# Kernel tuning notes

Measured on AMD Instinct MI355X. Metric: run time of the kernel, lower is better.

## Reference

```python
import jax, jax.numpy as jnp
import numpy as np

T, H, I, R, Z, K = 4096, 1024, 512, 32, 8, 4
E = R + Z
CAP = 768  # per-expert capacity; mean load = T*K/E = 409.6, CAP is ~18 sigma above mean


def setup_inputs() -> dict:
    key = jax.random.key(0)
    k1, k2, k3, k4, k5 = jax.random.split(key, 5)
    hidden_states = jax.random.normal(k1, (T, H), jnp.float32)
    top_k_index = jax.random.randint(k2, (T, K), 0, E).astype(jnp.int64)
    top_k_weights = jax.random.uniform(k3, (T, K), jnp.float32)
    gate_up_proj = jax.random.normal(k4, (E, 2 * I, H), jnp.float32) * 0.02
    down_proj = jax.random.normal(k5, (R, H, I), jnp.float32) * 0.02
    return {
        "hidden_states": hidden_states,
        "top_k_index": top_k_index,
        "top_k_weights": top_k_weights,
        "gate_up_proj": gate_up_proj,
        "down_proj": down_proj,
    }


def reference(hidden_states, top_k_index, top_k_weights, gate_up_proj, down_proj):
    n_tok, h = hidden_states.shape
    k = top_k_index.shape[1]
    n_routed = down_proj.shape[0]
    n_total = gate_up_proj.shape[0]
    A = n_tok * k  # total assignments

    flat_e = top_k_index.reshape(-1).astype(jnp.int32)          # [A]
    flat_t = jnp.repeat(jnp.arange(n_tok, dtype=jnp.int32), k)  # [A]
    flat_w = top_k_weights.reshape(-1)                          # [A]

    # ---- zero experts: weighted identity ----
    zero_w = jnp.sum(jnp.where(top_k_index >= n_routed, top_k_weights, 0.0), axis=1)
    out = hidden_states * zero_w[:, None]

    # ---- routed experts via capacity-buffer grouped GEMM ----
    order = jnp.argsort(flat_e)  # stable sort groups assignments by expert
    se = flat_e[order]
    st = flat_t[order]
    sw = flat_w[order]

    counts = jnp.bincount(flat_e, length=n_total)        # [E]
    starts = jnp.cumsum(counts) - counts                 # exclusive cumsum
    pos = jnp.arange(A, dtype=jnp.int32) - starts[se].astype(jnp.int32)  # slot within expert

    valid = (se < n_routed) & (pos < CAP)
    e_idx = jnp.where(valid, se, 0)
    p_idx = jnp.where(valid, pos, 0)

    xs = jnp.where(valid[:, None], hidden_states[st], 0.0)   # [A,H]
    xbuf = jnp.zeros((n_routed, CAP, h), hidden_states.dtype).at[e_idx, p_idx].add(xs)

    # grouped gated MLP: F.linear(x, W) == x @ W.T with W [out,in]
    gu = jnp.einsum('ech,eoh->eco', xbuf, gate_up_proj[:n_routed])  # [R,CAP,2I]
    gate, up = jnp.split(gu, 2, axis=-1)
    mid = jax.nn.silu(gate) * up                                    # [R,CAP,I]
    ybuf = jnp.einsum('eci,ehi->ech', mid, down_proj)               # [R,CAP,H]

    ya = ybuf[e_idx, p_idx] * jnp.where(valid, sw, 0.0)[:, None]    # [A,H]
    out = out.at[st].add(ya)
    return out
```

## Files before the change

kernel.cpp:

```cpp
#include <hip/hip_runtime.h>
#include <stdint.h>

#define NT 4096
#define HD 1024
#define ID 512
#define RE 32
#define EE 40
#define KT 4
#define CAPACITY 768

typedef __bf16 bf16x8 __attribute__((ext_vector_type(8)));
typedef float f32x4 __attribute__((ext_vector_type(4)));
typedef unsigned int u32x4 __attribute__((ext_vector_type(4)));
typedef unsigned short u16x4 __attribute__((ext_vector_type(4)));

__device__ __forceinline__ float bf2f(unsigned short u) {
    union { unsigned int i; float f; } v; v.i = ((unsigned int)u) << 16; return v.f;
}
__device__ __forceinline__ unsigned short f2bf(float f) {
    union { float f; unsigned int i; } v; v.f = f;
    unsigned int u = v.i;
    return (unsigned short)((u + 0x7fffu + ((u >> 16) & 1u)) >> 16);
}

__device__ __forceinline__ u32x4 ld8(const void* p, size_t ei, int inF32) {
    if (!inF32) {
        return *(const u32x4*)((const unsigned short*)p + ei);
    } else {
        const float* f = (const float*)p + ei;
        f32x4 a = *(const f32x4*)f;
        f32x4 b = *(const f32x4*)(f + 4);
        u32x4 r;
        r[0] = (unsigned)f2bf(a[0]) | ((unsigned)f2bf(a[1]) << 16);
        r[1] = (unsigned)f2bf(a[2]) | ((unsigned)f2bf(a[3]) << 16);
        r[2] = (unsigned)f2bf(b[0]) | ((unsigned)f2bf(b[1]) << 16);
        r[3] = (unsigned)f2bf(b[2]) | ((unsigned)f2bf(b[3]) << 16);
        return r;
    }
}

__global__ __launch_bounds__(256) void detect_k(const void* __restrict__ X,
                                                const void* __restrict__ idx,
                                                int* __restrict__ flags) {
    __shared__ int sInsane, sOddNZ;
    const int tid = threadIdx.x;
    if (tid == 0) { sInsane = 0; sOddNZ = 0; }
    __syncthreads();
    const unsigned short* xu = (const unsigned short*)X;
    int cnt = 0;
    for (int i = tid; i < 8192; i += 256) {
        int e = (xu[i] >> 7) & 0xFF;
        if (e >= 0x90) cnt++;
    }
    if (cnt) atomicAdd(&sInsane, cnt);
    const int* ip = (const int*)idx;
    int odd = 0;
    for (int i = tid; i < 512; i += 256)
        if ((i & 1) && ip[i] != 0) odd++;
    if (odd) atomicAdd(&sOddNZ, odd);
    __syncthreads();
    if (tid == 0) {
        flags[0] = (sInsane > 64) ? 1 : 0;
        flags[1] = (sOddNZ == 0) ? 1 : 0;
    }
}

__global__ __launch_bounds__(256) void route_k(const int* __restrict__ idx,
                                               const int* __restrict__ flags,
                                               int* __restrict__ cnt,
                                               int* __restrict__ tok,
                                               int* __restrict__ smap) {
    int a = blockIdx.x * 256 + threadIdx.x;
    if (a >= NT * KT) return;
    const int isI64 = flags[1];
    int e = isI64 ? idx[a << 1] : idx[a];
    int s = -1;
    if (e < RE) {
        int slot = atomicAdd(&cnt[e], 1);
        if (slot < CAPACITY) {
            tok[e * CAPACITY + slot] = a >> 2;
            s = slot;
        }
    }
    smap[a] = s;
}

__global__ __launch_bounds__(256, 2) void gemm1_k(
    const void* __restrict__ X,
    const void* __restrict__ W1,
    const int* __restrict__ flags,
    const int* __restrict__ cnts,
    const int* __restrict__ tok,
    unsigned short* __restrict__ mid)
{
    const int e = blockIdx.z;
    int cnt = cnts[e]; if (cnt > CAPACITY) cnt = CAPACITY;
    const int m0 = blockIdx.x * 128;
    if (m0 >= cnt) return;
    const int n0 = blockIdx.y * 128;
    const int inF32 = flags[0];

    __shared__ unsigned short Ash[4 * 128 * 8];
    __shared__ unsigned short Bgs[4 * 128 * 8];
    __shared__ unsigned short Bus[4 * 128 * 8];

    const int tid  = threadIdx.x;
    const int lane = tid & 63;
    const int wv   = tid >> 6;
    const int wm   = wv >> 1, wn = wv & 1;
    const int q    = lane >> 4, ln = lane & 15;

    const int row = tid & 127;
    const int kcb = tid >> 7;

    const int trow = (m0 + row < cnt) ? tok[e * CAPACITY + m0 + row] : 0;
    const size_t aOff = (size_t)trow * HD;
    const size_t gOff = ((size_t)e * 2 * ID + (n0 + row)) * HD;
    const size_t uOff = ((size_t)e * 2 * ID + (ID + n0 + row)) * HD;

    f32x4 accg[4][4], accu[4][4];
    const f32x4 z4 = {0.f, 0.f, 0.f, 0.f};
    #pragma unroll
    for (int a_ = 0; a_ < 4; a_++)
        #pragma unroll
        for (int b_ = 0; b_ < 4; b_++) { accg[a_][b_] = z4; accu[a_][b_] = z4; }

    u32x4 va[2], vg[2], vu[2];
    #pragma unroll
    for (int i = 0; i < 2; i++) {
        int kc = kcb + 2 * i;
        va[i] = ld8(X,  aOff + kc * 8, inF32);
        vg[i] = ld8(W1, gOff + kc * 8, inF32);
        vu[i] = ld8(W1, uOff + kc * 8, inF32);
    }

    for (int k0 = 0; k0 < HD; k0 += 32) {
        __syncthreads();
        #pragma unroll
        for (int i = 0; i < 2; i++) {
            int kc = kcb + 2 * i;
            *(u32x4*)&Ash[(kc * 128 + row) * 8] = va[i];
            *(u32x4*)&Bgs[(kc * 128 + row) * 8] = vg[i];
            *(u32x4*)&Bus[(kc * 128 + row) * 8] = vu[i];
        }
        __syncthreads();
        if (k0 + 32 < HD) {
            #pragma unroll
            for (int i = 0; i < 2; i++) {
                int kc = kcb + 2 * i;
                va[i] = ld8(X,  aOff + k0 + 32 + kc * 8, inF32);
                vg[i] = ld8(W1, gOff + k0 + 32 + kc * 8, inF32);
                vu[i] = ld8(W1, uOff + k0 + 32 + kc * 8, inF32);
            }
        }
        bf16x8 af[4], bgf[4], buf2[4];
        #pragma unroll
        for (int mt = 0; mt < 4; mt++)
            af[mt] = *(const bf16x8*)&Ash[(q * 128 + wm * 64 + mt * 16 + ln) * 8];
        #pragma unroll
        for (int nt = 0; nt < 4; nt++) {
            bgf[nt]  = *(const bf16x8*)&Bgs[(q * 128 + wn * 64 + nt * 16 + ln) * 8];
            buf2[nt] = *(const bf16x8*)&Bus[(q * 128 + wn * 64 + nt * 16 + ln) * 8];
        }
        #pragma unroll
        for (int mt = 0; mt < 4; mt++)
            #pragma unroll
            for (int nt = 0; nt < 4; nt++) {
                accg[mt][nt] = __builtin_amdgcn_mfma_f32_16x16x32_bf16(af[mt], bgf[nt],  accg[mt][nt], 0, 0, 0);
                accu[mt][nt] = __builtin_amdgcn_mfma_f32_16x16x32_bf16(af[mt], buf2[nt], accu[mt][nt], 0, 0, 0);
            }
    }

    const size_t midBase = (size_t)e * CAPACITY;
    #pragma unroll
    for (int mt = 0; mt < 4; mt++) {
        #pragma unroll
        for (int r = 0; r < 4; r++) {
            int slot = m0 + wm * 64 + mt * 16 + q * 4 + r;
            if (slot < cnt) {
                unsigned short* dst = mid + (midBase + slot) * ID;
                #pragma unroll
                for (int nt = 0; nt < 4; nt++) {
                    int i_col = n0 + wn * 64 + nt * 16 + ln;
                    float gv = accg[mt][nt][r];
                    float uv = accu[mt][nt][r];
                    float sv = gv / (1.f + __expf(-gv));
                    dst[i_col] = f2bf(sv * uv);
                }
            }
        }
    }
}

__global__ __launch_bounds__(256, 2) void gemm2_k(
    const unsigned short* __restrict__ mid,
    const void* __restrict__ W2,
    const int* __restrict__ flags,
    const int* __restrict__ cnts,
    unsigned short* __restrict__ ybuf)
{
    const int e = blockIdx.z;
    int cnt = cnts[e]; if (cnt > CAPACITY) cnt = CAPACITY;
    const int m0 = blockIdx.x * 128;
    if (m0 >= cnt) return;
    const int n0 = blockIdx.y * 128;
    const int inF32 = flags[0];

    __shared__ unsigned short Ash[4 * 128 * 8];
    __shared__ unsigned short Bsh[4 * 128 * 8];

    const int tid  = threadIdx.x;
    const int lane = tid & 63;
    const int wv   = tid >> 6;
    const int wm   = wv >> 1, wn = wv & 1;
    const int q    = lane >> 4, ln = lane & 15;

    const int row = tid & 127;
    const int kcb = tid >> 7;

    const unsigned short* aBase = mid + ((size_t)e * CAPACITY + m0 + row) * ID;
    const size_t bOff = ((size_t)e * HD + n0 + row) * ID;

    f32x4 acc[4][4];
    const f32x4 z4 = {0.f, 0.f, 0.f, 0.f};
    #pragma unroll
    for (int a_ = 0; a_ < 4; a_++)
        #pragma unroll
        for (int b_ = 0; b_ < 4; b_++) acc[a_][b_] = z4;

    u32x4 va[2], vb[2];
    #pragma unroll
    for (int i = 0; i < 2; i++) {
        int kc = kcb + 2 * i;
        va[i] = *(const u32x4*)(aBase + kc * 8);
        vb[i] = ld8(W2, bOff + kc * 8, inF32);
    }

    for (int k0 = 0; k0 < ID; k0 += 32) {
        __syncthreads();
        #pragma unroll
        for (int i = 0; i < 2; i++) {
            int kc = kcb + 2 * i;
            *(u32x4*)&Ash[(kc * 128 + row) * 8] = va[i];
            *(u32x4*)&Bsh[(kc * 128 + row) * 8] = vb[i];
        }
        __syncthreads();
        if (k0 + 32 < ID) {
            #pragma unroll
            for (int i = 0; i < 2; i++) {
                int kc = kcb + 2 * i;
                va[i] = *(const u32x4*)(aBase + k0 + 32 + kc * 8);
                vb[i] = ld8(W2, bOff + k0 + 32 + kc * 8, inF32);
            }
        }
        bf16x8 af[4], bf[4];
        #pragma unroll
        for (int mt = 0; mt < 4; mt++)
            af[mt] = *(const bf16x8*)&Ash[(q * 128 + wm * 64 + mt * 16 + ln) * 8];
        #pragma unroll
        for (int nt = 0; nt < 4; nt++)
            bf[nt] = *(const bf16x8*)&Bsh[(q * 128 + wn * 64 + nt * 16 + ln) * 8];
        #pragma unroll
        for (int mt = 0; mt < 4; mt++)
            #pragma unroll
            for (int nt = 0; nt < 4; nt++)
                acc[mt][nt] = __builtin_amdgcn_mfma_f32_16x16x32_bf16(af[mt], bf[nt], acc[mt][nt], 0, 0, 0);
    }

    const size_t yBase = (size_t)e * CAPACITY;
    #pragma unroll
    for (int mt = 0; mt < 4; mt++) {
        #pragma unroll
        for (int r = 0; r < 4; r++) {
            int slot = m0 + wm * 64 + mt * 16 + q * 4 + r;
            if (slot < cnt) {
                unsigned short* dst = ybuf + (yBase + slot) * HD;
                #pragma unroll
                for (int nt = 0; nt < 4; nt++) {
                    int h = n0 + wn * 64 + nt * 16 + ln;
                    dst[h] = f2bf(acc[mt][nt][r]);
                }
            }
        }
    }
}

__global__ __launch_bounds__(256) void gather_k(
    const void* __restrict__ X,
    const int* __restrict__ idx,
    const void* __restrict__ wts,
    const int* __restrict__ flags,
    const int* __restrict__ smap,
    const unsigned short* __restrict__ ybuf,
    float* __restrict__ out)
{
    const int t = blockIdx.x;
    const int tid = threadIdx.x;
    const int inF32 = flags[0];
    __shared__ int se[KT];
    __shared__ float sw[KT];
    __shared__ int ss[KT];
    if (tid < KT) {
        const int isI64 = flags[1];
        int a = t * KT + tid;
        se[tid] = isI64 ? idx[a << 1] : idx[a];
        sw[tid] = inF32 ? ((const float*)wts)[a] : bf2f(((const unsigned short*)wts)[a]);
        ss[tid] = smap[a];
    }
    __syncthreads();

    const int h = tid * 4;
    float x0, x1, x2, x3;
    if (inF32) {
        f32x4 xv = *(const f32x4*)((const float*)X + (size_t)t * HD + h);
        x0 = xv[0]; x1 = xv[1]; x2 = xv[2]; x3 = xv[3];
    } else {
        u16x4 xv = *(const u16x4*)((const unsigned short*)X + (size_t)t * HD + h);
        x0 = bf2f(xv[0]); x1 = bf2f(xv[1]); x2 = bf2f(xv[2]); x3 = bf2f(xv[3]);
    }
    float zw = 0.f;
    #pragma unroll
    for (int k = 0; k < KT; k++)
        if (se[k] >= RE) zw += sw[k];

    float a0 = zw * x0, a1 = zw * x1, a2 = zw * x2, a3 = zw * x3;

    #pragma unroll
    for (int k = 0; k < KT; k++) {
        if (se[k] < RE && ss[k] >= 0) {
            u16x4 yv = *(const u16x4*)&ybuf[((size_t)se[k] * CAPACITY + ss[k]) * HD + h];
            float w = sw[k];
            a0 += w * bf2f(yv[0]);
            a1 += w * bf2f(yv[1]);
            a2 += w * bf2f(yv[2]);
            a3 += w * bf2f(yv[3]);
        }
    }
    f32x4 o = {a0, a1, a2, a3};
    *(f32x4*)&out[(size_t)t * HD + h] = o;
}

extern "C" void kernel_launch(void* const* d_in, const int* in_sizes, int n_in,
                              void* d_out, int out_size, void* d_ws, size_t ws_size,
                              hipStream_t stream) {
    (void)in_sizes; (void)n_in; (void)out_size; (void)ws_size;
    const void* X   = d_in[0];
    const int*  idx = (const int*)d_in[1];
    const void* wts = d_in[2];
    const void* W1  = d_in[3];
    const void* W2  = d_in[4];
    float* out = (float*)d_out;

    char* ws = (char*)d_ws;
    int* flags = (int*)ws;
    int* cnt   = (int*)(ws + 128);
    int* tok   = (int*)(ws + 256);
    int* smap  = (int*)(ws + 256 + 98304);
    unsigned short* mid  = (unsigned short*)(ws + 164224);
    unsigned short* ybuf = (unsigned short*)(ws + 164224 + 25165824);

    hipMemsetAsync(ws, 0, 256, stream);
    detect_k<<<dim3(1), dim3(256), 0, stream>>>(X, idx, flags);
    route_k<<<dim3(64), dim3(256), 0, stream>>>(idx, flags, cnt, tok, smap);
    gemm1_k<<<dim3(6, 4, 32), dim3(256), 0, stream>>>(X, W1, flags, cnt, tok, mid);
    gemm2_k<<<dim3(6, 8, 32), dim3(256), 0, stream>>>(mid, W2, flags, cnt, ybuf);
    gather_k<<<dim3(4096), dim3(256), 0, stream>>>(X, idx, wts, flags, smap, ybuf, out);
}
```

Measured before the change: 587.2 us.

## Pre-convert inputs to bf16 and stage GEMM tiles via global_load_lds

Adds a conversion kernel that writes bf16 copies of X, W1 and W2 into the workspace. New GEMM kernels then load tiles straight into LDS with global_load_lds instead of going through registers. This is meant to remove the fp32 loads and conversions inside the GEMM inner loops, at the cost of one extra full pass over the weights each call. The new path only runs when the workspace is large enough, and ybuf reuses the W1b region after gemm1 finishes.

Result: faster. 493.5 us (-16.0%).

```diff
diff --git a/kernel.cpp b/kernel.cpp
--- a/kernel.cpp
+++ b/kernel.cpp
@@ -12,6 +12,7 @@
 typedef __bf16 bf16x8 __attribute__((ext_vector_type(8)));
 typedef float f32x4 __attribute__((ext_vector_type(4)));
 typedef unsigned int u32x4 __attribute__((ext_vector_type(4)));
+typedef unsigned int u32x2 __attribute__((ext_vector_type(2)));
 typedef unsigned short u16x4 __attribute__((ext_vector_type(4)));
 
 __device__ __forceinline__ float bf2f(unsigned short u) {
@@ -38,6 +39,10 @@
         return r;
     }
 }
+
+typedef __attribute__((address_space(1))) const unsigned int gas_u32;
+typedef __attribute__((address_space(3))) unsigned int las_u32;
+#define GLL(g, l) __builtin_amdgcn_global_load_lds((gas_u32*)(g), (las_u32*)(l), 16, 0, 0)
 
 __global__ __launch_bounds__(256) void detect_k(const void* __restrict__ X,
                                                 const void* __restrict__ idx,
@@ -85,10 +90,47 @@
     smap[a] = s;
 }
 
-__global__ __launch_bounds__(256, 2) void gemm1_k(
-    const void* __restrict__ X,
-    const void* __restrict__ W1,
+__global__ __launch_bounds__(256) void convert_k(
+    const void* __restrict__ X, const void* __restrict__ W1, const void* __restrict__ W2,
     const int* __restrict__ flags,
+    unsigned short* __restrict__ Xb, unsigned short* __restrict__ W1b,
+    unsigned short* __restrict__ W2b)
+{
+    const int inF32 = flags[0];
+    const size_t gid = (size_t)blockIdx.x * 256 + threadIdx.x;
+    const size_t stride = (size_t)gridDim.x * 256;
+    const size_t nx = (size_t)NT * HD / 4;
+    const size_t n1 = (size_t)RE * 2 * ID * HD / 4;
+    const size_t n2 = (size_t)RE * HD * ID / 4;
+    if (inF32) {
+        for (size_t i = gid; i < nx; i += stride) {
+            f32x4 v = ((const f32x4*)X)[i];
+            u32x2 r; r[0] = (unsigned)f2bf(v[0]) | ((unsigned)f2bf(v[1]) << 16);
+            r[1] = (unsigned)f2bf(v[2]) | ((unsigned)f2bf(v[3]) << 16);
+            ((u32x2*)Xb)[i] = r;
+        }
+        for (size_t i = gid; i < n1; i += stride) {
+            f32x4 v = ((const f32x4*)W1)[i];
+            u32x2 r; r[0] = (unsigned)f2bf(v[0]) | ((unsigned)f2bf(v[1]) << 16);
+            r[1] = (unsigned)f2bf(v[2]) | ((unsigned)f2bf(v[3]) << 16);
+            ((u32x2*)W1b)[i] = r;
+        }
+        for (size_t i = gid; i < n2; i += stride) {
+            f32x4 v = ((const f32x4*)W2)[i];
+            u32x2 r; r[0] = (unsigned)f2bf(v[0]) | ((unsigned)f2bf(v[1]) << 16);
+            r[1] = (unsigned)f2bf(v[2]) | ((unsigned)f2bf(v[3]) << 16);
+            ((u32x2*)W2b)[i] = r;
+        }
+    } else {
+        for (size_t i = gid; i < nx; i += stride) ((u32x2*)Xb)[i] = ((const u32x2*)X)[i];
+        for (size_t i = gid; i < n1; i += stride) ((u32x2*)W1b)[i] = ((const u32x2*)W1)[i];
+        for (size_t i = gid; i < n2; i += stride) ((u32x2*)W2b)[i] = ((const u32x2*)W2)[i];
+    }
+}
+
+__global__ __launch_bounds__(256, 2) void gemm1n_k(
+    const unsigned short* __restrict__ Xb,
+    const unsigned short* __restrict__ W1b,
     const int* __restrict__ cnts,
     const int* __restrict__ tok,
     unsigned short* __restrict__ mid)
@@ -98,7 +140,6 @@
     const int m0 = blockIdx.x * 128;
     if (m0 >= cnt) return;
     const int n0 = blockIdx.y * 128;
-    const int inF32 = flags[0];
 
     __shared__ unsigned short Ash[4 * 128 * 8];
     __shared__ unsigned short Bgs[4 * 128 * 8];
@@ -110,13 +151,21 @@
     const int wm   = wv >> 1, wn = wv & 1;
     const int q    = lane >> 4, ln = lane & 15;
 
-    const int row = tid & 127;
-    const int kcb = tid >> 7;
-
-    const int trow = (m0 + row < cnt) ? tok[e * CAPACITY + m0 + row] : 0;
-    const size_t aOff = (size_t)trow * HD;
-    const size_t gOff = ((size_t)e * 2 * ID + (n0 + row)) * HD;
-    const size_t uOff = ((size_t)e * 2 * ID + (ID + n0 + row)) * HD;
+    const int r0 = m0 + lane, r1 = m0 + 64 + lane;
+    const int t0 = (r0 < cnt) ? tok[e * CAPACITY + r0] : 0;
+    const int t1 = (r1 < cnt) ? tok[e * CAPACITY + r1] : 0;
+    const unsigned short* gA0 = Xb + (size_t)t0 * HD + wv * 8;
+    const unsigned short* gA1 = Xb + (size_t)t1 * HD + wv * 8;
+    const unsigned short* gG0 = W1b + ((size_t)e * 1024 + n0 + lane) * HD + wv * 8;
+    const unsigned short* gG1 = gG0 + (size_t)64 * HD;
+    const unsigned short* gU0 = W1b + ((size_t)e * 1024 + 512 + n0 + lane) * HD + wv * 8;
+    const unsigned short* gU1 = gU0 + (size_t)64 * HD;
+    unsigned short* lA0 = &Ash[(wv * 128 + 0) * 8];
+    unsigned short* lA1 = &Ash[(wv * 128 + 64) * 8];
+    unsigned short* lG0 = &Bgs[(wv * 128 + 0) * 8];
+    unsigned short* lG1 = &Bgs[(wv * 128 + 64) * 8];
+    unsigned short* lU0 = &Bus[(wv * 128 + 0) * 8];
+    unsigned short* lU1 = &Bus[(wv * 128 + 64) * 8];
 
     f32x4 accg[4][4], accu[4][4];
     const f32x4 z4 = {0.f, 0.f, 0.f, 0.f};
@@ -125,34 +174,14 @@
         #pragma unroll
         for (int b_ = 0; b_ < 4; b_++) { accg[a_][b_] = z4; accu[a_][b_] = z4; }
 
-    u32x4 va[2], vg[2], vu[2];
-    #pragma unroll
-    for (int i = 0; i < 2; i++) {
-        int kc = kcb + 2 * i;
-        va[i] = ld8(X,  aOff + kc * 8, inF32);
-        vg[i] = ld8(W1, gOff + kc * 8, inF32);
-        vu[i] = ld8(W1, uOff + kc * 8, inF32);
-    }
-
+    #define STAGE1(k0) do { \
+        GLL(gA0 + (k0), lA0); GLL(gA1 + (k0), lA1); \
+        GLL(gG0 + (k0), lG0); GLL(gG1 + (k0), lG1); \
+        GLL(gU0 + (k0), lU0); GLL(gU1 + (k0), lU1); } while (0)
+
+    STAGE1(0);
     for (int k0 = 0; k0 < HD; k0 += 32) {
         __syncthreads();
-        #pragma unroll
-        for (int i = 0; i < 2; i++) {
-            int kc = kcb + 2 * i;
-            *(u32x4*)&Ash[(kc * 128 + row) * 8] = va[i];
-            *(u32x4*)&Bgs[(kc * 128 + row) * 8] = vg[i];
-            *(u32x4*)&Bus[(kc * 128 + row) * 8] = vu[i];
-        }
-        __syncthreads();
-        if (k0 + 32 < HD) {
-            #pragma unroll
-            for (int i = 0; i < 2; i++) {
-                int kc = kcb + 2 * i;
-                va[i] = ld8(X,  aOff + k0 + 32 + kc * 8, inF32);
-                vg[i] = ld8(W1, gOff + k0 + 32 + kc * 8, inF32);
-                vu[i] = ld8(W1, uOff + k0 + 32 + kc * 8, inF32);
-            }
-        }
         bf16x8 af[4], bgf[4], buf2[4];
         #pragma unroll
         for (int mt = 0; mt < 4; mt++)
@@ -162,6 +191,8 @@
             bgf[nt]  = *(const bf16x8*)&Bgs[(q * 128 + wn * 64 + nt * 16 + ln) * 8];
             buf2[nt] = *(const bf16x8*)&Bus[(q * 128 + wn * 64 + nt * 16 + ln) * 8];
         }
+        __syncthreads();
+        if (k0 + 32 < HD) STAGE1(k0 + 32);
         #pragma unroll
         for (int mt = 0; mt < 4; mt++)
             #pragma unroll
@@ -170,6 +201,7 @@
                 accu[mt][nt] = __builtin_amdgcn_mfma_f32_16x16x32_bf16(af[mt], buf2[nt], accu[mt][nt], 0, 0, 0);
             }
     }
+    #undef STAGE1
 
     const size_t midBase = (size_t)e * CAPACITY;
     #pragma unroll
@@ -192,10 +224,9 @@
     }
 }
 
-__global__ __launch_bounds__(256, 2) void gemm2_k(
+__global__ __launch_bounds__(256, 2) void gemm2n_k(
     const unsigned short* __restrict__ mid,
-    const void* __restrict__ W2,
-    const int* __restrict__ flags,
+    const unsigned short* __restrict__ W2b,
     const int* __restrict__ cnts,
     unsigned short* __restrict__ ybuf)
 {
@@ -204,7 +235,6 @@
     const int m0 = blockIdx.x * 128;
     if (m0 >= cnt) return;
     const int n0 = blockIdx.y * 128;
-    const int inF32 = flags[0];
 
     __shared__ unsigned short Ash[4 * 128 * 8];
     __shared__ unsigned short Bsh[4 * 128 * 8];
@@ -215,6 +245,187 @@
     const int wm   = wv >> 1, wn = wv & 1;
     const int q    = lane >> 4, ln = lane & 15;
 
+    const unsigned short* gA0 = mid + ((size_t)e * CAPACITY + m0 + lane) * ID + wv * 8;
+    const unsigned short* gA1 = gA0 + (size_t)64 * ID;
+    const unsigned short* gB0 = W2b + ((size_t)e * HD + n0 + lane) * ID + wv * 8;
+    const unsigned short* gB1 = gB0 + (size_t)64 * ID;
+    unsigned short* lA0 = &Ash[(wv * 128 + 0) * 8];
+    unsigned short* lA1 = &Ash[(wv * 128 + 64) * 8];
+    unsigned short* lB0 = &Bsh[(wv * 128 + 0) * 8];
+    unsigned short* lB1 = &Bsh[(wv * 128 + 64) * 8];
+
+    f32x4 acc[4][4];
+    const f32x4 z4 = {0.f, 0.f, 0.f, 0.f};
+    #pragma unroll
+    for (int a_ = 0; a_ < 4; a_++)
+        #pragma unroll
+        for (int b_ = 0; b_ < 4; b_++) acc[a_][b_] = z4;
+
+    #define STAGE2(k0) do { \
+        GLL(gA0 + (k0), lA0); GLL(gA1 + (k0), lA1); \
+        GLL(gB0 + (k0), lB0); GLL(gB1 + (k0), lB1); } while (0)
+
+    STAGE2(0);
+    for (int k0 = 0; k0 < ID; k0 += 32) {
+        __syncthreads();
+        bf16x8 af[4], bf[4];
+        #pragma unroll
+        for (int mt = 0; mt < 4; mt++)
+            af[mt] = *(const bf16x8*)&Ash[(q * 128 + wm * 64 + mt * 16 + ln) * 8];
+        #pragma unroll
+        for (int nt = 0; nt < 4; nt++)
+            bf[nt] = *(const bf16x8*)&Bsh[(q * 128 + wn * 64 + nt * 16 + ln) * 8];
+        __syncthreads();
+        if (k0 + 32 < ID) STAGE2(k0 + 32);
+        #pragma unroll
+        for (int mt = 0; mt < 4; mt++)
+            #pragma unroll
+            for (int nt = 0; nt < 4; nt++)
+                acc[mt][nt] = __builtin_amdgcn_mfma_f32_16x16x32_bf16(af[mt], bf[nt], acc[mt][nt], 0, 0, 0);
+    }
+    #undef STAGE2
+
+    const size_t yBase = (size_t)e * CAPACITY;
+    #pragma unroll
+    for (int mt = 0; mt < 4; mt++) {
+        #pragma unroll
+        for (int r = 0; r < 4; r++) {
+            int slot = m0 + wm * 64 + mt * 16 + q * 4 + r;
+            if (slot < cnt) {
+                unsigned short* dst = ybuf + (yBase + slot) * HD;
+                #pragma unroll
+                for (int nt = 0; nt < 4; nt++) {
+                    int h = n0 + wn * 64 + nt * 16 + ln;
+                    dst[h] = f2bf(acc[mt][nt][r]);
+                }
+            }
+        }
+    }
+}
+
+__global__ __launch_bounds__(256, 2) void gemm1_k(
+    const void* __restrict__ X, const void* __restrict__ W1,
+    const int* __restrict__ flags, const int* __restrict__ cnts,
+    const int* __restrict__ tok, unsigned short* __restrict__ mid)
+{
+    const int e = blockIdx.z;
+    int cnt = cnts[e]; if (cnt > CAPACITY) cnt = CAPACITY;
+    const int m0 = blockIdx.x * 128;
+    if (m0 >= cnt) return;
+    const int n0 = blockIdx.y * 128;
+    const int inF32 = flags[0];
+
+    __shared__ unsigned short Ash[4 * 128 * 8];
+    __shared__ unsigned short Bgs[4 * 128 * 8];
+    __shared__ unsigned short Bus[4 * 128 * 8];
+
+    const int tid  = threadIdx.x;
+    const int lane = tid & 63;
+    const int wv   = tid >> 6;
+    const int wm   = wv >> 1, wn = wv & 1;
+    const int q    = lane >> 4, ln = lane & 15;
+    const int row = tid & 127;
+    const int kcb = tid >> 7;
+
+    const int trow = (m0 + row < cnt) ? tok[e * CAPACITY + m0 + row] : 0;
+    const size_t aOff = (size_t)trow * HD;
+    const size_t gOff = ((size_t)e * 2 * ID + (n0 + row)) * HD;
+    const size_t uOff = ((size_t)e * 2 * ID + (ID + n0 + row)) * HD;
+
+    f32x4 accg[4][4], accu[4][4];
+    const f32x4 z4 = {0.f, 0.f, 0.f, 0.f};
+    #pragma unroll
+    for (int a_ = 0; a_ < 4; a_++)
+        #pragma unroll
+        for (int b_ = 0; b_ < 4; b_++) { accg[a_][b_] = z4; accu[a_][b_] = z4; }
+
+    u32x4 va[2], vg[2], vu[2];
+    #pragma unroll
+    for (int i = 0; i < 2; i++) {
+        int kc = kcb + 2 * i;
+        va[i] = ld8(X,  aOff + kc * 8, inF32);
+        vg[i] = ld8(W1, gOff + kc * 8, inF32);
+        vu[i] = ld8(W1, uOff + kc * 8, inF32);
+    }
+
+    for (int k0 = 0; k0 < HD; k0 += 32) {
+        __syncthreads();
+        #pragma unroll
+        for (int i = 0; i < 2; i++) {
+            int kc = kcb + 2 * i;
+            *(u32x4*)&Ash[(kc * 128 + row) * 8] = va[i];
+            *(u32x4*)&Bgs[(kc * 128 + row) * 8] = vg[i];
+            *(u32x4*)&Bus[(kc * 128 + row) * 8] = vu[i];
+        }
+        __syncthreads();
+        if (k0 + 32 < HD) {
+            #pragma unroll
+            for (int i = 0; i < 2; i++) {
+                int kc = kcb + 2 * i;
+                va[i] = ld8(X,  aOff + k0 + 32 + kc * 8, inF32);
+                vg[i] = ld8(W1, gOff + k0 + 32 + kc * 8, inF32);
+                vu[i] = ld8(W1, uOff + k0 + 32 + kc * 8, inF32);
+            }
+        }
+        bf16x8 af[4], bgf[4], buf2[4];
+        #pragma unroll
+        for (int mt = 0; mt < 4; mt++)
+            af[mt] = *(const bf16x8*)&Ash[(q * 128 + wm * 64 + mt * 16 + ln) * 8];
+        #pragma unroll
+        for (int nt = 0; nt < 4; nt++) {
+            bgf[nt]  = *(const bf16x8*)&Bgs[(q * 128 + wn * 64 + nt * 16 + ln) * 8];
+            buf2[nt] = *(const bf16x8*)&Bus[(q * 128 + wn * 64 + nt * 16 + ln) * 8];
+        }
+        #pragma unroll
+        for (int mt = 0; mt < 4; mt++)
+            #pragma unroll
+            for (int nt = 0; nt < 4; nt++) {
+                accg[mt][nt] = __builtin_amdgcn_mfma_f32_16x16x32_bf16(af[mt], bgf[nt],  accg[mt][nt], 0, 0, 0);
+                accu[mt][nt] = __builtin_amdgcn_mfma_f32_16x16x32_bf16(af[mt], buf2[nt], accu[mt][nt], 0, 0, 0);
+            }
+    }
+
+    const size_t midBase = (size_t)e * CAPACITY;
+    #pragma unroll
+    for (int mt = 0; mt < 4; mt++) {
+        #pragma unroll
+        for (int r = 0; r < 4; r++) {
+            int slot = m0 + wm * 64 + mt * 16 + q * 4 + r;
+            if (slot < cnt) {
+                unsigned short* dst = mid + (midBase + slot) * ID;
+                #pragma unroll
+                for (int nt = 0; nt < 4; nt++) {
+                    int i_col = n0 + wn * 64 + nt * 16 + ln;
+                    float gv = accg[mt][nt][r];
+                    float uv = accu[mt][nt][r];
+                    float sv = gv / (1.f + __expf(-gv));
+                    dst[i_col] = f2bf(sv * uv);
+                }
+            }
+        }
+    }
+}
+
+__global__ __launch_bounds__(256, 2) void gemm2_k(
+    const unsigned short* __restrict__ mid, const void* __restrict__ W2,
+    const int* __restrict__ flags, const int* __restrict__ cnts,
+    unsigned short* __restrict__ ybuf)
+{
+    const int e = blockIdx.z;
+    int cnt = cnts[e]; if (cnt > CAPACITY) cnt = CAPACITY;
+    const int m0 = blockIdx.x * 128;
+    if (m0 >= cnt) return;
+    const int n0 = blockIdx.y * 128;
+    const int inF32 = flags[0];
+
+    __shared__ unsigned short Ash[4 * 128 * 8];
+    __shared__ unsigned short Bsh[4 * 128 * 8];
+
+    const int tid  = threadIdx.x;
+    const int lane = tid & 63;
+    const int wv   = tid >> 6;
+    const int wm   = wv >> 1, wn = wv & 1;
+    const int q    = lane >> 4, ln = lane & 15;
     const int row = tid & 127;
     const int kcb = tid >> 7;
 
@@ -343,7 +554,7 @@
 extern "C" void kernel_launch(void* const* d_in, const int* in_sizes, int n_in,
                               void* d_out, int out_size, void* d_ws, size_t ws_size,
                               hipStream_t stream) {
-    (void)in_sizes; (void)n_in; (void)out_size; (void)ws_size;
+    (void)in_sizes; (void)n_in; (void)out_size;
     const void* X   = d_in[0];
     const int*  idx = (const int*)d_in[1];
     const void* wts = d_in[2];
@@ -356,13 +567,31 @@
     int* cnt   = (int*)(ws + 128);
     int* tok   = (int*)(ws + 256);
     int* smap  = (int*)(ws + 256 + 98304);
-    unsigned short* mid  = (unsigned short*)(ws + 164224);
-    unsigned short* ybuf = (unsigned short*)(ws + 164224 + 25165824);
+    unsigned short* mid = (unsigned short*)(ws + 164224);
+
+    const size_t MIDE = 164224ull + 25165824ull;
+    const size_t W2BO = MIDE;
+    const size_t XBO  = W2BO + 33554432ull;
+    const size_t W1BO = XBO + 8388608ull;
+    const size_t NEED = W1BO + 67108864ull;
 
     hipMemsetAsync(ws, 0, 256, stream);
     detect_k<<<dim3(1), dim3(256), 0, stream>>>(X, idx, flags);
     route_k<<<dim3(64), dim3(256), 0, stream>>>(idx, flags, cnt, tok, smap);
-    gemm1_k<<<dim3(6, 4, 32), dim3(256), 0, stream>>>(X, W1, flags, cnt, tok, mid);
-    gemm2_k<<<dim3(6, 8, 32), dim3(256), 0, stream>>>(mid, W2, flags, cnt, ybuf);
-    gather_k<<<dim3(4096), dim3(256), 0, stream>>>(X, idx, wts, flags, smap, ybuf, out);
-}
+
+    if (ws_size >= NEED) {
+        unsigned short* W2b  = (unsigned short*)(ws + W2BO);
+        unsigned short* Xb   = (unsigned short*)(ws + XBO);
+        unsigned short* W1b  = (unsigned short*)(ws + W1BO);
+        unsigned short* ybuf = (unsigned short*)(ws + W1BO);
+        convert_k<<<dim3(2048), dim3(256), 0, stream>>>(X, W1, W2, flags, Xb, W1b, W2b);
+        gemm1n_k<<<dim3(6, 4, 32), dim3(256), 0, stream>>>(Xb, W1b, cnt, tok, mid);
+        gemm2n_k<<<dim3(6, 8, 32), dim3(256), 0, stream>>>(mid, W2b, cnt, ybuf);
+        gather_k<<<dim3(4096), dim3(256), 0, stream>>>(X, idx, wts, flags, smap, ybuf, out);
+    } else {
+        unsigned short* ybuf = (unsigned short*)(ws + 164224 + 25165824);
+        gemm1_k<<<dim3(6, 4, 32), dim3(256), 0, stream>>>(X, W1, flags, cnt, tok, mid);
+        gemm2_k<<<dim3(6, 8, 32), dim3(256), 0, stream>>>(mid, W2, flags, cnt, ybuf);
+        gather_k<<<dim3(4096), dim3(256), 0, stream>>>(X, idx, wts, flags, smap, ybuf, out);
+    }
+}
```
